# Optimization experiments

Hardware: AMD Instinct MI355X
Metric: run time of the kernel (lower is better)

The kernel has to match this reference:

```python
import jax, jax.numpy as jnp
import numpy as np

N_NODES = 100000
N_EDGES = 1600000
NUM_GRAPHS = 1000

def gcn_conv(x, edge_index, W, b, n):
    # PyG GCNConv: out = D^-1/2 (A + I) D^-1/2 (x W) + b
    xw = x @ W                                   # [n, F_out]
    loop = jnp.arange(n, dtype=edge_index.dtype)
    src = jnp.concatenate([edge_index[0], loop])  # sources (messages come from src)
    dst = jnp.concatenate([edge_index[1], loop])  # targets (aggregated into dst)
    deg = jnp.zeros((n,), xw.dtype).at[dst].add(1.0)
    dinv = jnp.where(deg > 0, jax.lax.rsqrt(deg), 0.0)
    norm = dinv[src] * dinv[dst]                  # [E+n]
    msg = xw[src] * norm[:, None]                 # gather + scale
    out = jax.ops.segment_sum(msg, dst, num_segments=n)
    return out + b

def scatter_mean(x, seg, num_segments):
    sums = jax.ops.segment_sum(x, seg, num_segments=num_segments)
    cnt = jax.ops.segment_sum(jnp.ones((x.shape[0],), x.dtype), seg, num_segments=num_segments)
    return sums / jnp.maximum(cnt, 1.0)[:, None]

def setup_inputs() -> dict:
    key = jax.random.key(0)
    ks = jax.random.split(key, 9)
    x = jax.random.normal(ks[0], (N_NODES, 256), dtype=jnp.float32)
    edge_index = jax.random.randint(ks[1], (2, N_EDGES), 0, N_NODES, dtype=jnp.int64 if jax.config.jax_enable_x64 else jnp.int32).astype(jnp.int32)
    batch = jnp.sort(jax.random.randint(ks[2], (N_NODES,), 0, NUM_GRAPHS)).astype(jnp.int32)
    W1 = jax.random.normal(ks[3], (256, 128), dtype=jnp.float32) * 0.05
    b1 = jax.random.normal(ks[4], (128,), dtype=jnp.float32) * 0.05
    W2 = jax.random.normal(ks[5], (128, 64), dtype=jnp.float32) * 0.05
    b2 = jax.random.normal(ks[6], (64,), dtype=jnp.float32) * 0.05
    fc_W = jax.random.normal(ks[7], (64, 4), dtype=jnp.float32) * 0.05
    fc_b = jax.random.normal(ks[8], (4,), dtype=jnp.float32) * 0.05
    return {"x": x, "edge_index": edge_index, "batch": batch, "W1": W1, "b1": b1, "W2": W2, "b2": b2, "fc_W": fc_W, "fc_b": fc_b}

def reference(x, edge_index, batch, W1, b1, W2, b2, fc_W, fc_b):
    n = x.shape[0]
    h = gcn_conv(x, edge_index, W1, b1, n)
    h = jax.nn.relu(h)                 # dropout p=0.0 is identity
    h = gcn_conv(h, edge_index, W2, b2, n)
    g = scatter_mean(h, batch, NUM_GRAPHS)   # [G, out_feats]
    logits = g @ fc_W + fc_b
    return jax.nn.log_softmax(logits, axis=1)
```

## Files before the change

kernel.cpp:

```cpp
#include <hip/hip_runtime.h>
#include <hip/hip_bf16.h>

#define N_NODES 100000
#define N_EDGES 1600000
#define NUM_GRAPHS 1000

#define NODES_PER_BUCKET 256
#define BUCKET_SHIFT 8
#define NBUCKETS 391
#define CAP 5120

#define G1_BLOCKS 1563
#define FUSED_BLOCKS 2345
#define FILL_CHUNK 2052

typedef __attribute__((ext_vector_type(8))) short short8;
typedef __attribute__((ext_vector_type(4))) float f32x4;
typedef __attribute__((ext_vector_type(2))) float f32x2;
typedef unsigned short ushort;

__device__ __forceinline__ ushort f2bf(float f) {
    unsigned int u = __float_as_uint(f);
    u = u + 0x7fffu + ((u >> 16) & 1u);
    return (ushort)(u >> 16);
}

__device__ __forceinline__ unsigned char f2fp8(float f) {
    return (unsigned char)(__builtin_amdgcn_cvt_pk_fp8_f32(f, f, 0, false) & 0xff);
}

__global__ void setup_kernel(int* __restrict__ bcursor,
                             const float* __restrict__ W1, ushort* __restrict__ W1t,
                             const float* __restrict__ W2, ushort* __restrict__ W2t,
                             float* __restrict__ gsum, float* __restrict__ gcnt) {
    int b = blockIdx.x, tid = threadIdx.x;
    if (b < 2) {
        int i = b * 256 + tid;
        if (i < NBUCKETS) bcursor[i] = i * CAP;
    } else if (b < 130) {
        int idx = (b - 2) * 256 + tid;
        int n = idx & 127, k = idx >> 7;
        W1t[n * 256 + k] = f2bf(W1[k * 128 + n]);
    } else if (b < 162) {
        int idx = (b - 130) * 256 + tid;
        int n = idx & 63, k = idx >> 6;
        W2t[n * 128 + k] = f2bf(W2[k * 64 + n]);
    } else {
        int idx = (b - 162) * 256 + tid;
        if (idx < NUM_GRAPHS * 64) gsum[idx] = 0.f;
        else if (idx < NUM_GRAPHS * 64 + NUM_GRAPHS) gcnt[idx - NUM_GRAPHS * 64] = 0.f;
    }
}
#define SETUP_BLOCKS 416

__global__ __launch_bounds__(256) void gemm1_fill_kernel(const float* __restrict__ x,
                                                         const ushort* __restrict__ W1t,
                                                         unsigned char* __restrict__ outb,
                                                         const int* __restrict__ esrc,
                                                         const int* __restrict__ edst,
                                                         int* __restrict__ bcursor,
                                                         int* __restrict__ pairs) {
    __shared__ short8 Bs[2048];
    const int b = blockIdx.x;
    const int tid = threadIdx.x;

    if (b % 3 == 2) {
        int* scnt = (int*)Bs;
        int* spos = scnt + NBUCKETS;
        const int fid = b / 3;
        const int beg = fid * FILL_CHUNK;
        int end = beg + FILL_CHUNK;
        if (end > N_EDGES) end = N_EDGES;
        if (beg >= end) return;
        for (int i = tid; i < NBUCKETS; i += 256) scnt[i] = 0;
        __syncthreads();
        for (int e = beg + tid * 4; e < end; e += 1024) {
            int4 d4 = *(const int4*)&edst[e];
            atomicAdd(&scnt[d4.x >> BUCKET_SHIFT], 1);
            atomicAdd(&scnt[d4.y >> BUCKET_SHIFT], 1);
            atomicAdd(&scnt[d4.z >> BUCKET_SHIFT], 1);
            atomicAdd(&scnt[d4.w >> BUCKET_SHIFT], 1);
        }
        __syncthreads();
        for (int i = tid; i < NBUCKETS; i += 256) {
            int c = scnt[i];
            spos[i] = c > 0 ? atomicAdd(&bcursor[i], c) : 0;
        }
        __syncthreads();
        for (int e = beg + tid * 4; e < end; e += 1024) {
            int4 d4 = *(const int4*)&edst[e];
            int4 s4 = *(const int4*)&esrc[e];
            int p0 = atomicAdd(&spos[d4.x >> BUCKET_SHIFT], 1);
            pairs[p0] = (s4.x << 8) | (d4.x & 255);
            int p1 = atomicAdd(&spos[d4.y >> BUCKET_SHIFT], 1);
            pairs[p1] = (s4.y << 8) | (d4.y & 255);
            int p2 = atomicAdd(&spos[d4.z >> BUCKET_SHIFT], 1);
            pairs[p2] = (s4.z << 8) | (d4.z & 255);
            int p3 = atomicAdd(&spos[d4.w >> BUCKET_SHIFT], 1);
            pairs[p3] = (s4.w << 8) | (d4.w & 255);
        }
        return;
    }

    const int gid = b - (b + 1) / 3;
    if (gid >= G1_BLOCKS) return;
    const int row0 = gid * 64;
    const int wv = tid >> 6;
    const int l = tid & 63;
    const int lrow = l & 15;
    const int quad = l >> 4;

    int r0 = row0 + wv * 16 + lrow;
    if (r0 > N_NODES - 1) r0 = N_NODES - 1;
    const float* xr0 = x + (size_t)r0 * 256 + quad * 8;
    const int frag = lrow * 4 + quad;

    f32x4 acc[8];
#pragma unroll
    for (int t = 0; t < 8; ++t) acc[t] = (f32x4){0.f, 0.f, 0.f, 0.f};

    for (int s = 0; s < 2; ++s) {
        if (s) __syncthreads();
#pragma unroll
        for (int j = 0; j < 8; ++j) {
            int slot = j * 256 + tid;
            int kcl = slot >> 9, t = (slot >> 6) & 7, lr = (slot >> 2) & 15, q = slot & 3;
            Bs[slot] = *(const short8*)(W1t + (t * 16 + lr) * 256 + (s * 4 + kcl) * 32 + q * 8);
        }
        __syncthreads();

#pragma unroll
        for (int kcl = 0; kcl < 4; ++kcl) {
            const int kc = s * 4 + kcl;
            float4 a00 = *(const float4*)(xr0 + kc * 32);
            float4 a01 = *(const float4*)(xr0 + kc * 32 + 4);
            short8 af0;
            af0[0] = (short)f2bf(a00.x); af0[1] = (short)f2bf(a00.y);
            af0[2] = (short)f2bf(a00.z); af0[3] = (short)f2bf(a00.w);
            af0[4] = (short)f2bf(a01.x); af0[5] = (short)f2bf(a01.y);
            af0[6] = (short)f2bf(a01.z); af0[7] = (short)f2bf(a01.w);
#pragma unroll
            for (int t = 0; t < 8; ++t) {
                short8 bfrag = Bs[kcl * 512 + t * 64 + frag];
                acc[t] = __builtin_amdgcn_mfma_f32_16x16x32_bf16(af0, bfrag, acc[t], 0, 0, 0);
            }
        }
    }

    const int rbase = row0 + wv * 16 + quad * 4;
#pragma unroll
    for (int t = 0; t < 8; ++t) {
#pragma unroll
        for (int r = 0; r < 4; ++r) {
            int row = rbase + r;
            if (row < N_NODES)
                outb[(size_t)row * 128 + t * 16 + lrow] = f2fp8(acc[t][r]);
        }
    }
}

__global__ __launch_bounds__(256) void csr_fill_local_kernel(const int* __restrict__ pairs,
                                                             const int* __restrict__ bcursor,
                                                             int* __restrict__ csr_src,
                                                             int* __restrict__ row_beg,
                                                             int* __restrict__ row_end,
                                                             float* __restrict__ dinv) {
    __shared__ int plds[CAP];
    __shared__ int hist[256];
    __shared__ int scanv[256];
    __shared__ int cur[256];
    const int b = blockIdx.x;
    const int base = b * CAP;
    const int tid = threadIdx.x;
    const int cnt_b = bcursor[b] - base;

    for (int i = tid; i < cnt_b; i += 256) plds[i] = pairs[base + i];
    hist[tid] = 0;
    __syncthreads();
    for (int i = tid; i < cnt_b; i += 256) atomicAdd(&hist[plds[i] & 255], 1);
    __syncthreads();

    int deg = hist[tid];
    scanv[tid] = deg;
    for (int off = 1; off < 256; off <<= 1) {
        __syncthreads();
        int add = (tid >= off) ? scanv[tid - off] : 0;
        __syncthreads();
        scanv[tid] += add;
    }
    __syncthreads();
    int excl = scanv[tid] - deg;

    int node = b * NODES_PER_BUCKET + tid;
    if (node < N_NODES) {
        int beg = base + excl;
        row_beg[node] = beg;
        row_end[node] = beg + deg;
        dinv[node] = rsqrtf((float)(deg + 1));
    }
    cur[tid] = excl;
    __syncthreads();

    for (int i = tid; i < cnt_b; i += 256) {
        int pr = plds[i];
        int pos = base + atomicAdd(&cur[pr & 255], 1);
        csr_src[pos] = ((unsigned int)pr) >> 8;
    }
}

__global__ __launch_bounds__(256) void agg1_kernel(const unsigned int* __restrict__ xw,
                                                   const int* __restrict__ csr_src,
                                                   const int* __restrict__ row_beg,
                                                   const int* __restrict__ row_end,
                                                   const float* __restrict__ dinv,
                                                   const float* __restrict__ bias,
                                                   ushort* __restrict__ h) {
    const int wave = threadIdx.x >> 6;
    const int lane = threadIdx.x & 63;
    const int h2 = lane >> 5;
    const int c = lane & 31;
    const int node = blockIdx.x * 8 + wave * 2 + h2;

    const int beg = row_beg[node], end = row_end[node];
    const float dvn = rsqrtf((float)(end - beg + 1));

    unsigned int sv = xw[(size_t)node * 32 + c];
    f32x2 slo = __builtin_amdgcn_cvt_pk_f32_fp8(sv, false);
    f32x2 shi = __builtin_amdgcn_cvt_pk_f32_fp8(sv, true);
    float a0 = dvn * slo[0], a1 = dvn * slo[1], a2 = dvn * shi[0], a3 = dvn * shi[1];

    for (int e = beg; e < end; e += 16) {
        int s[16];
        s[0] = csr_src[e];
#pragma unroll
        for (int i = 1; i < 16; ++i)
            s[i] = (e + i < end) ? csr_src[e + i] : s[0];
        unsigned int v[16];
        float ds[16];
#pragma unroll
        for (int i = 0; i < 16; ++i) {
            v[i] = xw[(size_t)s[i] * 32 + c];
            ds[i] = dinv[s[i]];
        }
#pragma unroll
        for (int i = 0; i < 16; ++i) {
            if (i == 0 || e + i < end) {
                f32x2 lo = __builtin_amdgcn_cvt_pk_f32_fp8(v[i], false);
                f32x2 hi = __builtin_amdgcn_cvt_pk_f32_fp8(v[i], true);
                a0 += ds[i] * lo[0]; a1 += ds[i] * lo[1];
                a2 += ds[i] * hi[0]; a3 += ds[i] * hi[1];
            }
        }
    }
    float4 bv = *(const float4*)&bias[c * 4];
    float v0 = a0 * dvn + bv.x, v1 = a1 * dvn + bv.y;
    float v2 = a2 * dvn + bv.z, v3 = a3 * dvn + bv.w;
    ushort4 o;
    o.x = f2bf(v0 > 0.f ? v0 : 0.f);
    o.y = f2bf(v1 > 0.f ? v1 : 0.f);
    o.z = f2bf(v2 > 0.f ? v2 : 0.f);
    o.w = f2bf(v3 > 0.f ? v3 : 0.f);
    *(ushort4*)&h[(size_t)node * 128 + c * 4] = o;
}

__global__ __launch_bounds__(256) void gemm2_kernel(const ushort* __restrict__ h,
                                                    const ushort* __restrict__ W2t,
                                                    unsigned char* __restrict__ outb) {
    __shared__ short8 Bs[1024];
    const int tid = threadIdx.x;
    const int row0 = blockIdx.x * 128;
    const int wv = tid >> 6;
    const int l = tid & 63;
    const int lrow = l & 15;
    const int quad = l >> 4;

    int r0 = row0 + wv * 16 + lrow;
    int r1 = r0 + 64;
    if (r0 > N_NODES - 1) r0 = N_NODES - 1;
    if (r1 > N_NODES - 1) r1 = N_NODES - 1;
    const ushort* h0 = h + (size_t)r0 * 128 + quad * 8;
    const ushort* h1 = h + (size_t)r1 * 128 + quad * 8;
    const int frag = lrow * 4 + quad;

#pragma unroll
    for (int j = 0; j < 4; ++j) {
        int slot = j * 256 + tid;
        int kc = slot >> 8, t = (slot >> 6) & 3, lr = (slot >> 2) & 15, q = slot & 3;
        Bs[slot] = *(const short8*)(W2t + (t * 16 + lr) * 128 + kc * 32 + q * 8);
    }
    __syncthreads();

    f32x4 acc[2][4];
#pragma unroll
    for (int m = 0; m < 2; ++m)
#pragma unroll
        for (int t = 0; t < 4; ++t) acc[m][t] = (f32x4){0.f, 0.f, 0.f, 0.f};

#pragma unroll
    for (int kc = 0; kc < 4; ++kc) {
        short8 af0 = *(const short8*)(h0 + kc * 32);
        short8 af1 = *(const short8*)(h1 + kc * 32);
#pragma unroll
        for (int t = 0; t < 4; ++t) {
            short8 bfrag = Bs[kc * 256 + t * 64 + frag];
            acc[0][t] = __builtin_amdgcn_mfma_f32_16x16x32_bf16(af0, bfrag, acc[0][t], 0, 0, 0);
            acc[1][t] = __builtin_amdgcn_mfma_f32_16x16x32_bf16(af1, bfrag, acc[1][t], 0, 0, 0);
        }
    }

#pragma unroll
    for (int m = 0; m < 2; ++m) {
        const int rbase = row0 + m * 64 + wv * 16 + quad * 4;
#pragma unroll
        for (int r = 0; r < 4; ++r) {
            int row = rbase + r;
            if (row < N_NODES) {
#pragma unroll
                for (int t = 0; t < 4; ++t)
                    outb[(size_t)row * 64 + t * 16 + lrow] = f2fp8(acc[m][t][r]);
            }
        }
    }
}

__global__ __launch_bounds__(256) void agg2_pool_kernel(const unsigned int* __restrict__ xw,
                                                        const int* __restrict__ csr_src,
                                                        const int* __restrict__ row_beg,
                                                        const int* __restrict__ row_end,
                                                        const float* __restrict__ dinv,
                                                        const float* __restrict__ bias,
                                                        const int* __restrict__ batch,
                                                        float* __restrict__ gsum,
                                                        float* __restrict__ gcnt) {
    __shared__ float part[16][64];
    __shared__ int bsh[16];
    const int wave = threadIdx.x >> 6;
    const int lane = threadIdx.x & 63;
    const int q = lane >> 4;
    const int c = lane & 15;
    const int nl = wave * 4 + q;
    const int node = blockIdx.x * 16 + nl;

    const int beg = row_beg[node], end = row_end[node];
    const float dvn = rsqrtf((float)(end - beg + 1));

    unsigned int sv = xw[(size_t)node * 16 + c];
    f32x2 slo = __builtin_amdgcn_cvt_pk_f32_fp8(sv, false);
    f32x2 shi = __builtin_amdgcn_cvt_pk_f32_fp8(sv, true);
    float a0 = dvn * slo[0], a1 = dvn * slo[1], a2 = dvn * shi[0], a3 = dvn * shi[1];

    for (int e = beg; e < end; e += 16) {
        int s[16];
        s[0] = csr_src[e];
#pragma unroll
        for (int i = 1; i < 16; ++i)
            s[i] = (e + i < end) ? csr_src[e + i] : s[0];
        unsigned int v[16];
        float ds[16];
#pragma unroll
        for (int i = 0; i < 16; ++i) {
            v[i] = xw[(size_t)s[i] * 16 + c];
            ds[i] = dinv[s[i]];
        }
#pragma unroll
        for (int i = 0; i < 16; ++i) {
            if (i == 0 || e + i < end) {
                f32x2 lo = __builtin_amdgcn_cvt_pk_f32_fp8(v[i], false);
                f32x2 hi = __builtin_amdgcn_cvt_pk_f32_fp8(v[i], true);
                a0 += ds[i] * lo[0]; a1 += ds[i] * lo[1];
                a2 += ds[i] * hi[0]; a3 += ds[i] * hi[1];
            }
        }
    }
    float4 bv = *(const float4*)&bias[c * 4];
    float4 val = make_float4(a0 * dvn + bv.x, a1 * dvn + bv.y,
                             a2 * dvn + bv.z, a3 * dvn + bv.w);
    *(float4*)&part[nl][c * 4] = val;
    if (lane == (q << 4)) bsh[nl] = batch[node];
    __syncthreads();

    if (wave == 0) {
        int b0 = bsh[0];
        bool same = true;
#pragma unroll
        for (int i = 1; i < 16; ++i) same = same && (bsh[i] == b0);
        if (same) {
            float s = 0.f;
#pragma unroll
            for (int i = 0; i < 16; ++i) s += part[i][lane];
            atomicAdd(&gsum[b0 * 64 + lane], s);
            if (lane == 0) atomicAdd(&gcnt[b0], 16.0f);
        } else {
#pragma unroll
            for (int i = 0; i < 16; ++i)
                atomicAdd(&gsum[bsh[i] * 64 + lane], part[i][lane]);
            if (lane == 0) {
#pragma unroll
                for (int i = 0; i < 16; ++i) atomicAdd(&gcnt[bsh[i]], 1.0f);
            }
        }
    }
}

__global__ void head_kernel(const float* __restrict__ gsum, const float* __restrict__ gcnt,
                            const float* __restrict__ fcW, const float* __restrict__ fcb,
                            float* __restrict__ out) {
    int g = blockIdx.x * blockDim.x + threadIdx.x;
    if (g >= NUM_GRAPHS) return;
    float c = gcnt[g];
    c = c > 1.f ? c : 1.f;
    float inv = 1.f / c;
    float logits[4];
#pragma unroll
    for (int j = 0; j < 4; ++j) logits[j] = fcb[j];
    for (int k = 0; k < 64; ++k) {
        float m = gsum[g * 64 + k] * inv;
#pragma unroll
        for (int j = 0; j < 4; ++j) logits[j] += m * fcW[k * 4 + j];
    }
    float mx = logits[0];
#pragma unroll
    for (int j = 1; j < 4; ++j) mx = logits[j] > mx ? logits[j] : mx;
    float s = 0.f;
#pragma unroll
    for (int j = 0; j < 4; ++j) s += expf(logits[j] - mx);
    float lse = mx + logf(s);
#pragma unroll
    for (int j = 0; j < 4; ++j) out[g * 4 + j] = logits[j] - lse;
}

extern "C" void kernel_launch(void* const* d_in, const int* in_sizes, int n_in,
                              void* d_out, int out_size, void* d_ws, size_t ws_size,
                              hipStream_t stream) {
    const float* x     = (const float*)d_in[0];
    const int*   ei    = (const int*)d_in[1];
    const int*   batch = (const int*)d_in[2];
    const float* W1    = (const float*)d_in[3];
    const float* b1    = (const float*)d_in[4];
    const float* W2    = (const float*)d_in[5];
    const float* b2    = (const float*)d_in[6];
    const float* fcW   = (const float*)d_in[7];
    const float* fcb   = (const float*)d_in[8];
    float* out = (float*)d_out;

    const int* src = ei;
    const int* dst = ei + N_EDGES;

    size_t o = 0;
    char* wsb = (char*)d_ws;
    auto take = [&](size_t bytes) -> void* {
        void* p = wsb + o;
        o += (bytes + 255) & ~(size_t)255;
        return p;
    };
    float* dinv      = (float*)take((size_t)N_NODES * 4);
    int*   row_beg   = (int*)take((size_t)N_NODES * 4);
    int*   row_end   = (int*)take((size_t)N_NODES * 4);
    int*   bcursor   = (int*)take((size_t)NBUCKETS * 4);
    int*   csr_src   = (int*)take((size_t)NBUCKETS * CAP * 4);
    int*   pairs     = (int*)take((size_t)NBUCKETS * CAP * 4);
    ushort* W1t      = (ushort*)take((size_t)128 * 256 * 2);
    ushort* W2t      = (ushort*)take((size_t)64 * 128 * 2);
    unsigned char* bufA = (unsigned char*)take((size_t)N_NODES * 128);
    ushort* bufB     = (ushort*)take((size_t)N_NODES * 128 * 2);
    float* gsum      = (float*)take((size_t)NUM_GRAPHS * 64 * 4);
    float* gcnt      = (float*)take((size_t)NUM_GRAPHS * 4);
    (void)ws_size;

    const int TB = 256;

    setup_kernel<<<SETUP_BLOCKS, TB, 0, stream>>>(bcursor, W1, W1t, W2, W2t, gsum, gcnt);

    gemm1_fill_kernel<<<FUSED_BLOCKS, TB, 0, stream>>>(x, W1t, bufA, src, dst, bcursor, pairs);

    csr_fill_local_kernel<<<NBUCKETS, TB, 0, stream>>>(pairs, bcursor, csr_src,
                                                       row_beg, row_end, dinv);

    agg1_kernel<<<N_NODES / 8, TB, 0, stream>>>((const unsigned int*)bufA, csr_src,
                                                row_beg, row_end, dinv, b1, bufB);

    gemm2_kernel<<<(N_NODES + 127) / 128, TB, 0, stream>>>(bufB, W2t, bufA);

    agg2_pool_kernel<<<N_NODES / 16, TB, 0, stream>>>((const unsigned int*)bufA, csr_src,
                                                      row_beg, row_end, dinv, b2, batch,
                                                      gsum, gcnt);

    head_kernel<<<(NUM_GRAPHS + TB - 1) / TB, TB, 0, stream>>>(gsum, gcnt, fcW, fcb, out);
}
```

Baseline: 308.0 us.

## Move CSR fill into gemm1 launch and run edge binning standalone

Splits the edge binning out of the fused gemm1 kernel into its own launch, and merges the per-bucket CSR fill into the gemm1 kernel as the first 391 blocks. The intent is to overlap the CSR construction with the dense GEMM rather than overlapping binning with it. The launch count stays the same. Binning now runs without overlap, and the CSR-fill blocks share a launch with GEMM blocks, which may change occupancy because the shared LDS buffer sizing is reused.

```diff
diff --git a/kernel.cpp b/kernel.cpp
--- a/kernel.cpp
+++ b/kernel.cpp
@@ -11,7 +11,8 @@
 #define CAP 5120
 
 #define G1_BLOCKS 1563
-#define FUSED_BLOCKS 2345
+#define GC_BLOCKS (391 + G1_BLOCKS)
+#define BIN_BLOCKS 781
 #define FILL_CHUNK 2052
 
 typedef __attribute__((ext_vector_type(8))) short short8;
@@ -53,57 +54,104 @@
 }
 #define SETUP_BLOCKS 416
 
-__global__ __launch_bounds__(256) void gemm1_fill_kernel(const float* __restrict__ x,
-                                                         const ushort* __restrict__ W1t,
-                                                         unsigned char* __restrict__ outb,
-                                                         const int* __restrict__ esrc,
-                                                         const int* __restrict__ edst,
-                                                         int* __restrict__ bcursor,
-                                                         int* __restrict__ pairs) {
+__global__ __launch_bounds__(256) void bin_kernel(const int* __restrict__ esrc,
+                                                  const int* __restrict__ edst,
+                                                  int* __restrict__ bcursor,
+                                                  int* __restrict__ pairs) {
+    __shared__ int scnt[NBUCKETS];
+    __shared__ int spos[NBUCKETS];
+    const int b = blockIdx.x;
+    const int tid = threadIdx.x;
+    const int beg = b * FILL_CHUNK;
+    int end = beg + FILL_CHUNK;
+    if (end > N_EDGES) end = N_EDGES;
+    if (beg >= end) return;
+    for (int i = tid; i < NBUCKETS; i += 256) scnt[i] = 0;
+    __syncthreads();
+    for (int e = beg + tid * 4; e < end; e += 1024) {
+        int4 d4 = *(const int4*)&edst[e];
+        atomicAdd(&scnt[d4.x >> BUCKET_SHIFT], 1);
+        atomicAdd(&scnt[d4.y >> BUCKET_SHIFT], 1);
+        atomicAdd(&scnt[d4.z >> BUCKET_SHIFT], 1);
+        atomicAdd(&scnt[d4.w >> BUCKET_SHIFT], 1);
+    }
+    __syncthreads();
+    for (int i = tid; i < NBUCKETS; i += 256) {
+        int c = scnt[i];
+        spos[i] = c > 0 ? atomicAdd(&bcursor[i], c) : 0;
+    }
+    __syncthreads();
+    for (int e = beg + tid * 4; e < end; e += 1024) {
+        int4 d4 = *(const int4*)&edst[e];
+        int4 s4 = *(const int4*)&esrc[e];
+        int p0 = atomicAdd(&spos[d4.x >> BUCKET_SHIFT], 1);
+        pairs[p0] = (s4.x << 8) | (d4.x & 255);
+        int p1 = atomicAdd(&spos[d4.y >> BUCKET_SHIFT], 1);
+        pairs[p1] = (s4.y << 8) | (d4.y & 255);
+        int p2 = atomicAdd(&spos[d4.z >> BUCKET_SHIFT], 1);
+        pairs[p2] = (s4.z << 8) | (d4.z & 255);
+        int p3 = atomicAdd(&spos[d4.w >> BUCKET_SHIFT], 1);
+        pairs[p3] = (s4.w << 8) | (d4.w & 255);
+    }
+}
+
+__global__ __launch_bounds__(256) void gemm1_csr_kernel(const float* __restrict__ x,
+                                                        const ushort* __restrict__ W1t,
+                                                        unsigned char* __restrict__ outb,
+                                                        const int* __restrict__ pairs,
+                                                        const int* __restrict__ bcursor,
+                                                        int* __restrict__ csr_src,
+                                                        int* __restrict__ row_beg,
+                                                        int* __restrict__ row_end,
+                                                        float* __restrict__ dinv) {
     __shared__ short8 Bs[2048];
     const int b = blockIdx.x;
     const int tid = threadIdx.x;
 
-    if (b % 3 == 2) {
-        int* scnt = (int*)Bs;
-        int* spos = scnt + NBUCKETS;
-        const int fid = b / 3;
-        const int beg = fid * FILL_CHUNK;
-        int end = beg + FILL_CHUNK;
-        if (end > N_EDGES) end = N_EDGES;
-        if (beg >= end) return;
-        for (int i = tid; i < NBUCKETS; i += 256) scnt[i] = 0;
+    if (b < NBUCKETS) {
+        int* plds  = (int*)Bs;
+        int* hist  = plds + CAP;
+        int* scanv = hist + 256;
+        int* cur   = scanv + 256;
+        const int base = b * CAP;
+        const int cnt_b = bcursor[b] - base;
+
+        for (int i = tid; i < cnt_b; i += 256) plds[i] = pairs[base + i];
+        hist[tid] = 0;
         __syncthreads();
-        for (int e = beg + tid * 4; e < end; e += 1024) {
-            int4 d4 = *(const int4*)&edst[e];
-            atomicAdd(&scnt[d4.x >> BUCKET_SHIFT], 1);
-            atomicAdd(&scnt[d4.y >> BUCKET_SHIFT], 1);
-            atomicAdd(&scnt[d4.z >> BUCKET_SHIFT], 1);
-            atomicAdd(&scnt[d4.w >> BUCKET_SHIFT], 1);
-        }
+        for (int i = tid; i < cnt_b; i += 256) atomicAdd(&hist[plds[i] & 255], 1);
         __syncthreads();
-        for (int i = tid; i < NBUCKETS; i += 256) {
-            int c = scnt[i];
-            spos[i] = c > 0 ? atomicAdd(&bcursor[i], c) : 0;
+
+        int deg = hist[tid];
+        scanv[tid] = deg;
+        for (int off = 1; off < 256; off <<= 1) {
+            __syncthreads();
+            int add = (tid >= off) ? scanv[tid - off] : 0;
+            __syncthreads();
+            scanv[tid] += add;
         }
         __syncthreads();
-        for (int e = beg + tid * 4; e < end; e += 1024) {
-            int4 d4 = *(const int4*)&edst[e];
-            int4 s4 = *(const int4*)&esrc[e];
-            int p0 = atomicAdd(&spos[d4.x >> BUCKET_SHIFT], 1);
-            pairs[p0] = (s4.x << 8) | (d4.x & 255);
-            int p1 = atomicAdd(&spos[d4.y >> BUCKET_SHIFT], 1);
-            pairs[p1] = (s4.y << 8) | (d4.y & 255);
-            int p2 = atomicAdd(&spos[d4.z >> BUCKET_SHIFT], 1);
-            pairs[p2] = (s4.z << 8) | (d4.z & 255);
-            int p3 = atomicAdd(&spos[d4.w >> BUCKET_SHIFT], 1);
-            pairs[p3] = (s4.w << 8) | (d4.w & 255);
+        int excl = scanv[tid] - deg;
+
+        int node = b * NODES_PER_BUCKET + tid;
+        if (node < N_NODES) {
+            int beg = base + excl;
+            row_beg[node] = beg;
+            row_end[node] = beg + deg;
+            dinv[node] = rsqrtf((float)(deg + 1));
+        }
+        cur[tid] = excl;
+        __syncthreads();
+
+        for (int i = tid; i < cnt_b; i += 256) {
+            int pr = plds[i];
+            int pos = base + atomicAdd(&cur[pr & 255], 1);
+            csr_src[pos] = ((unsigned int)pr) >> 8;
         }
         return;
     }
 
-    const int gid = b - (b + 1) / 3;
-    if (gid >= G1_BLOCKS) return;
+    const int gid = b - NBUCKETS;
     const int row0 = gid * 64;
     const int wv = tid >> 6;
     const int l = tid & 63;
@@ -156,55 +204,6 @@
             if (row < N_NODES)
                 outb[(size_t)row * 128 + t * 16 + lrow] = f2fp8(acc[t][r]);
         }
-    }
-}
-
-__global__ __launch_bounds__(256) void csr_fill_local_kernel(const int* __restrict__ pairs,
-                                                             const int* __restrict__ bcursor,
-                                                             int* __restrict__ csr_src,
-                                                             int* __restrict__ row_beg,
-                                                             int* __restrict__ row_end,
-                                                             float* __restrict__ dinv) {
-    __shared__ int plds[CAP];
-    __shared__ int hist[256];
-    __shared__ int scanv[256];
-    __shared__ int cur[256];
-    const int b = blockIdx.x;
-    const int base = b * CAP;
-    const int tid = threadIdx.x;
-    const int cnt_b = bcursor[b] - base;
-
-    for (int i = tid; i < cnt_b; i += 256) plds[i] = pairs[base + i];
-    hist[tid] = 0;
-    __syncthreads();
-    for (int i = tid; i < cnt_b; i += 256) atomicAdd(&hist[plds[i] & 255], 1);
-    __syncthreads();
-
-    int deg = hist[tid];
-    scanv[tid] = deg;
-    for (int off = 1; off < 256; off <<= 1) {
-        __syncthreads();
-        int add = (tid >= off) ? scanv[tid - off] : 0;
-        __syncthreads();
-        scanv[tid] += add;
-    }
-    __syncthreads();
-    int excl = scanv[tid] - deg;
-
-    int node = b * NODES_PER_BUCKET + tid;
-    if (node < N_NODES) {
-        int beg = base + excl;
-        row_beg[node] = beg;
-        row_end[node] = beg + deg;
-        dinv[node] = rsqrtf((float)(deg + 1));
-    }
-    cur[tid] = excl;
-    __syncthreads();
-
-    for (int i = tid; i < cnt_b; i += 256) {
-        int pr = plds[i];
-        int pos = base + atomicAdd(&cur[pr & 255], 1);
-        csr_src[pos] = ((unsigned int)pr) >> 8;
     }
 }
 
@@ -471,10 +470,10 @@
 
     setup_kernel<<<SETUP_BLOCKS, TB, 0, stream>>>(bcursor, W1, W1t, W2, W2t, gsum, gcnt);
 
-    gemm1_fill_kernel<<<FUSED_BLOCKS, TB, 0, stream>>>(x, W1t, bufA, src, dst, bcursor, pairs);
-
-    csr_fill_local_kernel<<<NBUCKETS, TB, 0, stream>>>(pairs, bcursor, csr_src,
-                                                       row_beg, row_end, dinv);
+    bin_kernel<<<BIN_BLOCKS, TB, 0, stream>>>(src, dst, bcursor, pairs);
+
+    gemm1_csr_kernel<<<GC_BLOCKS, TB, 0, stream>>>(x, W1t, bufA, pairs, bcursor,
+                                                   csr_src, row_beg, row_end, dinv);
 
     agg1_kernel<<<N_NODES / 8, TB, 0, stream>>>((const unsigned int*)bufA, csr_src,
                                                 row_beg, row_end, dinv, b1, bufB);
```

After: 316.2 us. 1.03x slower.

## Fuse layer-1 aggregation with layer-2 GEMM via swizzled LDS tile

Applied to the files above, without the earlier changes.

Merges the first-layer neighbor aggregation and the second-layer bf16 MFMA GEMM into one kernel. Each block aggregates 64 nodes into a shared-memory tile with an XOR swizzle, then multiplies that tile by W2 from LDS and writes fp8 output. This removes the bf16 hidden-feature round trip through global memory (about 25 MB) and one kernel launch. In exchange, per-block work is serialized over 8 iterations and the block count drops, which may reduce latency hiding in the gather-heavy aggregation.

```diff
diff --git a/kernel.cpp b/kernel.cpp
--- a/kernel.cpp
+++ b/kernel.cpp
@@ -208,117 +208,110 @@
     }
 }
 
-__global__ __launch_bounds__(256) void agg1_kernel(const unsigned int* __restrict__ xw,
-                                                   const int* __restrict__ csr_src,
-                                                   const int* __restrict__ row_beg,
-                                                   const int* __restrict__ row_end,
-                                                   const float* __restrict__ dinv,
-                                                   const float* __restrict__ bias,
-                                                   ushort* __restrict__ h) {
-    const int wave = threadIdx.x >> 6;
-    const int lane = threadIdx.x & 63;
+__global__ __launch_bounds__(256) void agg1_gemm2_kernel(const unsigned int* __restrict__ xw,
+                                                         const int* __restrict__ csr_src,
+                                                         const int* __restrict__ row_beg,
+                                                         const int* __restrict__ row_end,
+                                                         const float* __restrict__ dinv,
+                                                         const float* __restrict__ bias,
+                                                         const ushort* __restrict__ W2t,
+                                                         unsigned char* __restrict__ out2) {
+    __shared__ uint4 Hl4[1024];
+    __shared__ short8 Bs[1024];
+    unsigned char* Hl = (unsigned char*)Hl4;
+    const int tid = threadIdx.x;
+    const int wave = tid >> 6;
+    const int lane = tid & 63;
     const int h2 = lane >> 5;
     const int c = lane & 31;
-    const int node = blockIdx.x * 8 + wave * 2 + h2;
-
-    const int beg = row_beg[node], end = row_end[node];
-    const float dvn = rsqrtf((float)(end - beg + 1));
-
-    unsigned int sv = xw[(size_t)node * 32 + c];
-    f32x2 slo = __builtin_amdgcn_cvt_pk_f32_fp8(sv, false);
-    f32x2 shi = __builtin_amdgcn_cvt_pk_f32_fp8(sv, true);
-    float a0 = dvn * slo[0], a1 = dvn * slo[1], a2 = dvn * shi[0], a3 = dvn * shi[1];
-
-    for (int e = beg; e < end; e += 16) {
-        int s[16];
-        s[0] = csr_src[e];
-#pragma unroll
-        for (int i = 1; i < 16; ++i)
-            s[i] = (e + i < end) ? csr_src[e + i] : s[0];
-        unsigned int v[16];
-        float ds[16];
-#pragma unroll
-        for (int i = 0; i < 16; ++i) {
-            v[i] = xw[(size_t)s[i] * 32 + c];
-            ds[i] = dinv[s[i]];
-        }
-#pragma unroll
-        for (int i = 0; i < 16; ++i) {
-            if (i == 0 || e + i < end) {
-                f32x2 lo = __builtin_amdgcn_cvt_pk_f32_fp8(v[i], false);
-                f32x2 hi = __builtin_amdgcn_cvt_pk_f32_fp8(v[i], true);
-                a0 += ds[i] * lo[0]; a1 += ds[i] * lo[1];
-                a2 += ds[i] * hi[0]; a3 += ds[i] * hi[1];
+    const int node0 = blockIdx.x * 64;
+
+#pragma unroll
+    for (int j = 0; j < 4; ++j) {
+        int slot = j * 256 + tid;
+        int kc = slot >> 8, t = (slot >> 6) & 3, lr = (slot >> 2) & 15, q = slot & 3;
+        Bs[slot] = *(const short8*)(W2t + (t * 16 + lr) * 128 + kc * 32 + q * 8);
+    }
+
+    for (int it = 0; it < 8; ++it) {
+        const int row = it * 8 + wave * 2 + h2;
+        const int node = node0 + row;
+        float v0 = 0.f, v1 = 0.f, v2 = 0.f, v3 = 0.f;
+        if (node < N_NODES) {
+            const int beg = row_beg[node], end = row_end[node];
+            const float dvn = rsqrtf((float)(end - beg + 1));
+
+            unsigned int sv = xw[(size_t)node * 32 + c];
+            f32x2 slo = __builtin_amdgcn_cvt_pk_f32_fp8(sv, false);
+            f32x2 shi = __builtin_amdgcn_cvt_pk_f32_fp8(sv, true);
+            float a0 = dvn * slo[0], a1 = dvn * slo[1], a2 = dvn * shi[0], a3 = dvn * shi[1];
+
+            for (int e = beg; e < end; e += 16) {
+                int s[16];
+                s[0] = csr_src[e];
+#pragma unroll
+                for (int i = 1; i < 16; ++i)
+                    s[i] = (e + i < end) ? csr_src[e + i] : s[0];
+                unsigned int v[16];
+                float ds[16];
+#pragma unroll
+                for (int i = 0; i < 16; ++i) {
+                    v[i] = xw[(size_t)s[i] * 32 + c];
+                    ds[i] = dinv[s[i]];
+                }
+#pragma unroll
+                for (int i = 0; i < 16; ++i) {
+                    if (i == 0 || e + i < end) {
+                        f32x2 lo = __builtin_amdgcn_cvt_pk_f32_fp8(v[i], false);
+                        f32x2 hi = __builtin_amdgcn_cvt_pk_f32_fp8(v[i], true);
+                        a0 += ds[i] * lo[0]; a1 += ds[i] * lo[1];
+                        a2 += ds[i] * hi[0]; a3 += ds[i] * hi[1];
+                    }
+                }
             }
-        }
-    }
-    float4 bv = *(const float4*)&bias[c * 4];
-    float v0 = a0 * dvn + bv.x, v1 = a1 * dvn + bv.y;
-    float v2 = a2 * dvn + bv.z, v3 = a3 * dvn + bv.w;
-    ushort4 o;
-    o.x = f2bf(v0 > 0.f ? v0 : 0.f);
-    o.y = f2bf(v1 > 0.f ? v1 : 0.f);
-    o.z = f2bf(v2 > 0.f ? v2 : 0.f);
-    o.w = f2bf(v3 > 0.f ? v3 : 0.f);
-    *(ushort4*)&h[(size_t)node * 128 + c * 4] = o;
-}
-
-__global__ __launch_bounds__(256) void gemm2_kernel(const ushort* __restrict__ h,
-                                                    const ushort* __restrict__ W2t,
-                                                    unsigned char* __restrict__ outb) {
-    __shared__ short8 Bs[1024];
-    const int tid = threadIdx.x;
-    const int row0 = blockIdx.x * 128;
+            float4 bv = *(const float4*)&bias[c * 4];
+            v0 = a0 * dvn + bv.x; v1 = a1 * dvn + bv.y;
+            v2 = a2 * dvn + bv.z; v3 = a3 * dvn + bv.w;
+            v0 = v0 > 0.f ? v0 : 0.f;
+            v1 = v1 > 0.f ? v1 : 0.f;
+            v2 = v2 > 0.f ? v2 : 0.f;
+            v3 = v3 > 0.f ? v3 : 0.f;
+        }
+        ushort4 o;
+        o.x = f2bf(v0); o.y = f2bf(v1); o.z = f2bf(v2); o.w = f2bf(v3);
+        *(ushort4*)&Hl[((unsigned)(row * 256 + c * 8)) ^ (unsigned)((row & 7) << 4)] = o;
+    }
+    __syncthreads();
+
     const int wv = tid >> 6;
     const int l = tid & 63;
     const int lrow = l & 15;
     const int quad = l >> 4;
-
-    int r0 = row0 + wv * 16 + lrow;
-    int r1 = r0 + 64;
-    if (r0 > N_NODES - 1) r0 = N_NODES - 1;
-    if (r1 > N_NODES - 1) r1 = N_NODES - 1;
-    const ushort* h0 = h + (size_t)r0 * 128 + quad * 8;
-    const ushort* h1 = h + (size_t)r1 * 128 + quad * 8;
     const int frag = lrow * 4 + quad;
 
-#pragma unroll
-    for (int j = 0; j < 4; ++j) {
-        int slot = j * 256 + tid;
-        int kc = slot >> 8, t = (slot >> 6) & 3, lr = (slot >> 2) & 15, q = slot & 3;
-        Bs[slot] = *(const short8*)(W2t + (t * 16 + lr) * 128 + kc * 32 + q * 8);
-    }
-    __syncthreads();
-
-    f32x4 acc[2][4];
-#pragma unroll
-    for (int m = 0; m < 2; ++m)
-#pragma unroll
-        for (int t = 0; t < 4; ++t) acc[m][t] = (f32x4){0.f, 0.f, 0.f, 0.f};
+    f32x4 acc[4];
+#pragma unroll
+    for (int t = 0; t < 4; ++t) acc[t] = (f32x4){0.f, 0.f, 0.f, 0.f};
 
 #pragma unroll
     for (int kc = 0; kc < 4; ++kc) {
-        short8 af0 = *(const short8*)(h0 + kc * 32);
-        short8 af1 = *(const short8*)(h1 + kc * 32);
+        const int row = wv * 16 + lrow;
+        short8 af = *(const short8*)&Hl[((unsigned)(row * 256 + kc * 64 + quad * 16)) ^ (unsigned)((row & 7) << 4)];
 #pragma unroll
         for (int t = 0; t < 4; ++t) {
             short8 bfrag = Bs[kc * 256 + t * 64 + frag];
-            acc[0][t] = __builtin_amdgcn_mfma_f32_16x16x32_bf16(af0, bfrag, acc[0][t], 0, 0, 0);
-            acc[1][t] = __builtin_amdgcn_mfma_f32_16x16x32_bf16(af1, bfrag, acc[1][t], 0, 0, 0);
-        }
-    }
-
-#pragma unroll
-    for (int m = 0; m < 2; ++m) {
-        const int rbase = row0 + m * 64 + wv * 16 + quad * 4;
+            acc[t] = __builtin_amdgcn_mfma_f32_16x16x32_bf16(af, bfrag, acc[t], 0, 0, 0);
+        }
+    }
+
+    const int rbase = node0 + wv * 16 + quad * 4;
+#pragma unroll
+    for (int t = 0; t < 4; ++t) {
 #pragma unroll
         for (int r = 0; r < 4; ++r) {
             int row = rbase + r;
-            if (row < N_NODES) {
-#pragma unroll
-                for (int t = 0; t < 4; ++t)
-                    outb[(size_t)row * 64 + t * 16 + lrow] = f2fp8(acc[m][t][r]);
-            }
+            if (row < N_NODES)
+                out2[(size_t)row * 64 + t * 16 + lrow] = f2fp8(acc[t][r]);
         }
     }
 }
@@ -462,7 +455,7 @@
     ushort* W1t      = (ushort*)take((size_t)128 * 256 * 2);
     ushort* W2t      = (ushort*)take((size_t)64 * 128 * 2);
     unsigned char* bufA = (unsigned char*)take((size_t)N_NODES * 128);
-    ushort* bufB     = (ushort*)take((size_t)N_NODES * 128 * 2);
+    unsigned char* bufB = (unsigned char*)take((size_t)N_NODES * 64);
     float* gsum      = (float*)take((size_t)NUM_GRAPHS * 64 * 4);
     float* gcnt      = (float*)take((size_t)NUM_GRAPHS * 4);
     (void)ws_size;
@@ -476,12 +469,11 @@
     csr_fill_local_kernel<<<NBUCKETS, TB, 0, stream>>>(pairs, bcursor, csr_src,
                                                        row_beg, row_end, dinv);
 
-    agg1_kernel<<<N_NODES / 8, TB, 0, stream>>>((const unsigned int*)bufA, csr_src,
-                                                row_beg, row_end, dinv, b1, bufB);
-
-    gemm2_kernel<<<(N_NODES + 127) / 128, TB, 0, stream>>>(bufB, W2t, bufA);
-
-    agg2_pool_kernel<<<N_NODES / 16, TB, 0, stream>>>((const unsigned int*)bufA, csr_src,
+    agg1_gemm2_kernel<<<(N_NODES + 63) / 64, TB, 0, stream>>>((const unsigned int*)bufA, csr_src,
+                                                              row_beg, row_end, dinv, b1,
+                                                              W2t, bufB);
+
+    agg2_pool_kernel<<<N_NODES / 16, TB, 0, stream>>>((const unsigned int*)bufB, csr_src,
                                                       row_beg, row_end, dinv, b2, batch,
                                                       gsum, gcnt);
 
```

Result: slower. 330.6 us (+7.4%).

## Prescale source features by dinv to drop per-edge dinv gathers

Applied to the files above, without the earlier changes.

Source-side normalization dinv[src] is folded into the stored features before aggregation. For layer 2 it is applied in the gemm2 epilogue; for layer 1 a new scale pass runs after the CSR build, since dinv is not known during gemm1. As a result, gemm1 now writes bf16 to an intermediate buffer, and the new pass reads it, multiplies by dinv and repacks to fp8. This removes the random dinv gather per edge in both aggregation kernels, at the cost of an extra kernel launch and a 25.6 MB bf16 write plus read. The fp8 quantization also moves to after scaling, which slightly changes numerics.

```diff
diff --git a/kernel.cpp b/kernel.cpp
--- a/kernel.cpp
+++ b/kernel.cpp
@@ -23,6 +23,9 @@
     unsigned int u = __float_as_uint(f);
     u = u + 0x7fffu + ((u >> 16) & 1u);
     return (ushort)(u >> 16);
+}
+__device__ __forceinline__ float bf2f(ushort u) {
+    return __uint_as_float(((unsigned int)u) << 16);
 }
 
 __device__ __forceinline__ unsigned char f2fp8(float f) {
@@ -55,7 +58,7 @@
 
 __global__ __launch_bounds__(256) void gemm1_fill_kernel(const float* __restrict__ x,
                                                          const ushort* __restrict__ W1t,
-                                                         unsigned char* __restrict__ outb,
+                                                         ushort* __restrict__ outb,
                                                          const int* __restrict__ esrc,
                                                          const int* __restrict__ edst,
                                                          int* __restrict__ bcursor,
@@ -154,7 +157,7 @@
         for (int r = 0; r < 4; ++r) {
             int row = rbase + r;
             if (row < N_NODES)
-                outb[(size_t)row * 128 + t * 16 + lrow] = f2fp8(acc[t][r]);
+                outb[(size_t)row * 128 + t * 16 + lrow] = f2bf(acc[t][r]);
         }
     }
 }
@@ -208,11 +211,31 @@
     }
 }
 
+__global__ __launch_bounds__(256) void scale_kernel(const ushort* __restrict__ xwb,
+                                                    const float* __restrict__ dinv,
+                                                    unsigned int* __restrict__ outA) {
+    const int idx = blockIdx.x * 256 + threadIdx.x;
+    const int row = idx >> 4;
+    const int seg = idx & 15;
+    const float dv = dinv[row];
+    short8 v = *(const short8*)&xwb[(size_t)row * 128 + seg * 8];
+    float f0 = dv * bf2f((ushort)v[0]), f1 = dv * bf2f((ushort)v[1]);
+    float f2 = dv * bf2f((ushort)v[2]), f3 = dv * bf2f((ushort)v[3]);
+    float f4 = dv * bf2f((ushort)v[4]), f5 = dv * bf2f((ushort)v[5]);
+    float f6 = dv * bf2f((ushort)v[6]), f7 = dv * bf2f((ushort)v[7]);
+    unsigned int w0 = __builtin_amdgcn_cvt_pk_fp8_f32(f0, f1, 0, false);
+    w0 = __builtin_amdgcn_cvt_pk_fp8_f32(f2, f3, w0, true);
+    unsigned int w1 = __builtin_amdgcn_cvt_pk_fp8_f32(f4, f5, 0, false);
+    w1 = __builtin_amdgcn_cvt_pk_fp8_f32(f6, f7, w1, true);
+    outA[(size_t)row * 32 + seg * 2]     = w0;
+    outA[(size_t)row * 32 + seg * 2 + 1] = w1;
+}
+#define SCALE_BLOCKS 6250
+
 __global__ __launch_bounds__(256) void agg1_kernel(const unsigned int* __restrict__ xw,
                                                    const int* __restrict__ csr_src,
                                                    const int* __restrict__ row_beg,
                                                    const int* __restrict__ row_end,
-                                                   const float* __restrict__ dinv,
                                                    const float* __restrict__ bias,
                                                    ushort* __restrict__ h) {
     const int wave = threadIdx.x >> 6;
@@ -227,7 +250,7 @@
     unsigned int sv = xw[(size_t)node * 32 + c];
     f32x2 slo = __builtin_amdgcn_cvt_pk_f32_fp8(sv, false);
     f32x2 shi = __builtin_amdgcn_cvt_pk_f32_fp8(sv, true);
-    float a0 = dvn * slo[0], a1 = dvn * slo[1], a2 = dvn * shi[0], a3 = dvn * shi[1];
+    float a0 = slo[0], a1 = slo[1], a2 = shi[0], a3 = shi[1];
 
     for (int e = beg; e < end; e += 16) {
         int s[16];
@@ -236,19 +259,16 @@
         for (int i = 1; i < 16; ++i)
             s[i] = (e + i < end) ? csr_src[e + i] : s[0];
         unsigned int v[16];
-        float ds[16];
-#pragma unroll
-        for (int i = 0; i < 16; ++i) {
+#pragma unroll
+        for (int i = 0; i < 16; ++i)
             v[i] = xw[(size_t)s[i] * 32 + c];
-            ds[i] = dinv[s[i]];
-        }
 #pragma unroll
         for (int i = 0; i < 16; ++i) {
             if (i == 0 || e + i < end) {
                 f32x2 lo = __builtin_amdgcn_cvt_pk_f32_fp8(v[i], false);
                 f32x2 hi = __builtin_amdgcn_cvt_pk_f32_fp8(v[i], true);
-                a0 += ds[i] * lo[0]; a1 += ds[i] * lo[1];
-                a2 += ds[i] * hi[0]; a3 += ds[i] * hi[1];
+                a0 += lo[0]; a1 += lo[1];
+                a2 += hi[0]; a3 += hi[1];
             }
         }
     }
@@ -265,6 +285,7 @@
 
 __global__ __launch_bounds__(256) void gemm2_kernel(const ushort* __restrict__ h,
                                                     const ushort* __restrict__ W2t,
+                                                    const float* __restrict__ dinv,
                                                     unsigned char* __restrict__ outb) {
     __shared__ short8 Bs[1024];
     const int tid = threadIdx.x;
@@ -315,9 +336,10 @@
         for (int r = 0; r < 4; ++r) {
             int row = rbase + r;
             if (row < N_NODES) {
+                float dv = dinv[row];
 #pragma unroll
                 for (int t = 0; t < 4; ++t)
-                    outb[(size_t)row * 64 + t * 16 + lrow] = f2fp8(acc[m][t][r]);
+                    outb[(size_t)row * 64 + t * 16 + lrow] = f2fp8(dv * acc[m][t][r]);
             }
         }
     }
@@ -327,7 +349,6 @@
                                                         const int* __restrict__ csr_src,
                                                         const int* __restrict__ row_beg,
                                                         const int* __restrict__ row_end,
-                                                        const float* __restrict__ dinv,
                                                         const float* __restrict__ bias,
                                                         const int* __restrict__ batch,
                                                         float* __restrict__ gsum,
@@ -347,7 +368,7 @@
     unsigned int sv = xw[(size_t)node * 16 + c];
     f32x2 slo = __builtin_amdgcn_cvt_pk_f32_fp8(sv, false);
     f32x2 shi = __builtin_amdgcn_cvt_pk_f32_fp8(sv, true);
-    float a0 = dvn * slo[0], a1 = dvn * slo[1], a2 = dvn * shi[0], a3 = dvn * shi[1];
+    float a0 = slo[0], a1 = slo[1], a2 = shi[0], a3 = shi[1];
 
     for (int e = beg; e < end; e += 16) {
         int s[16];
@@ -356,19 +377,16 @@
         for (int i = 1; i < 16; ++i)
             s[i] = (e + i < end) ? csr_src[e + i] : s[0];
         unsigned int v[16];
-        float ds[16];
-#pragma unroll
-        for (int i = 0; i < 16; ++i) {
+#pragma unroll
+        for (int i = 0; i < 16; ++i)
             v[i] = xw[(size_t)s[i] * 16 + c];
-            ds[i] = dinv[s[i]];
-        }
 #pragma unroll
         for (int i = 0; i < 16; ++i) {
             if (i == 0 || e + i < end) {
                 f32x2 lo = __builtin_amdgcn_cvt_pk_f32_fp8(v[i], false);
                 f32x2 hi = __builtin_amdgcn_cvt_pk_f32_fp8(v[i], true);
-                a0 += ds[i] * lo[0]; a1 += ds[i] * lo[1];
-                a2 += ds[i] * hi[0]; a3 += ds[i] * hi[1];
+                a0 += lo[0]; a1 += lo[1];
+                a2 += hi[0]; a3 += hi[1];
             }
         }
     }
@@ -471,18 +489,20 @@
 
     setup_kernel<<<SETUP_BLOCKS, TB, 0, stream>>>(bcursor, W1, W1t, W2, W2t, gsum, gcnt);
 
-    gemm1_fill_kernel<<<FUSED_BLOCKS, TB, 0, stream>>>(x, W1t, bufA, src, dst, bcursor, pairs);
+    gemm1_fill_kernel<<<FUSED_BLOCKS, TB, 0, stream>>>(x, W1t, bufB, src, dst, bcursor, pairs);
 
     csr_fill_local_kernel<<<NBUCKETS, TB, 0, stream>>>(pairs, bcursor, csr_src,
                                                        row_beg, row_end, dinv);
 
+    scale_kernel<<<SCALE_BLOCKS, TB, 0, stream>>>(bufB, dinv, (unsigned int*)bufA);
+
     agg1_kernel<<<N_NODES / 8, TB, 0, stream>>>((const unsigned int*)bufA, csr_src,
-                                                row_beg, row_end, dinv, b1, bufB);
-
-    gemm2_kernel<<<(N_NODES + 127) / 128, TB, 0, stream>>>(bufB, W2t, bufA);
+                                                row_beg, row_end, b1, bufB);
+
+    gemm2_kernel<<<(N_NODES + 127) / 128, TB, 0, stream>>>(bufB, W2t, dinv, bufA);
 
     agg2_pool_kernel<<<N_NODES / 16, TB, 0, stream>>>((const unsigned int*)bufA, csr_src,
-                                                      row_beg, row_end, dinv, b2, batch,
+                                                      row_beg, row_end, b2, batch,
                                                       gsum, gcnt);
 
     head_kernel<<<(NUM_GRAPHS + TB - 1) / TB, TB, 0, stream>>>(gsum, gcnt, fcW, fcb, out);
```

Measured after the change: 309.3 us. No clear change (+0.4%).
